# Performance work log

Hardware: AMD Instinct MI355X
Metric: run time of the kernel (lower is better)

## Reference

```python
import jax, jax.numpy as jnp
import numpy as np

DT = 0.05

def _conv(x, w):
    # x: [N,C,H,W], w: [O,I,kh,kw], SAME padding
    return jax.lax.conv_general_dilated(x, w, (1, 1), 'SAME',
                                        dimension_numbers=('NCHW', 'OIHW', 'NCHW'))

def _gru(h, x, wx, wh):
    # convolutional GRU cell (used for Bayesian jumps and SpatialGRU)
    xr, xz, xg = jnp.split(_conv(x, wx), 3, axis=1)
    hr, hz, hg = jnp.split(_conv(h, wh), 3, axis=1)
    r = jax.nn.sigmoid(xr + hr)
    z = jax.nn.sigmoid(xz + hz)
    g = jnp.tanh(xg + r * hg)
    return (1.0 - z) * h + z * g

def _ode_step(h, wrz, wg, dt):
    # GRU-ODE cell, explicit Euler: dh/dt = (1-z)*(g-h)
    r, z = jnp.split(jax.nn.sigmoid(_conv(h, wrz)), 2, axis=1)
    g = jnp.tanh(_conv(r * h, wg))
    return h + dt * (1.0 - z) * (g - h)

def _sgru(x, h0, wx, wh):
    # SpatialGRU: conv-GRU recurrence over the sequence dim
    def step(h, xt):
        h = _gru(h, xt, wx, wh)
        return h, h
    _, hs = jax.lax.scan(step, h0, x.transpose(1, 0, 2, 3, 4))
    return hs.transpose(1, 0, 2, 3, 4)

def setup_inputs() -> dict:
    key = jax.random.key(0)
    B, C, H, W = 2, 64, 64, 64
    Nc, Nl, NF = 3, 5, 6
    ks = jax.random.split(key, 16)
    f = lambda i, s: jax.random.normal(ks[i], s, jnp.float32)
    w = lambda i, s: 0.05 * jax.random.normal(ks[i], s, jnp.float32)
    inp = {}
    inp['future_prediction_input'] = f(0, (B, C, H, W))
    inp['camera_states'] = f(1, (B, Nc, C, H, W))
    inp['lidar_states'] = f(2, (B, Nl, C, H, W))
    # ragged obs times as exact multiples of DT; targets after all obs
    inp['camera_timestamp'] = jnp.broadcast_to(jnp.array([0., 2., 4.]) * DT, (B, Nc)).astype(jnp.float32)
    inp['lidar_timestamp'] = jnp.broadcast_to(jnp.array([1., 3., 5., 6., 7.]) * DT, (B, Nl)).astype(jnp.float32)
    inp['target_timestamp'] = jnp.broadcast_to(jnp.arange(8., 14.) * DT, (B, NF)).astype(jnp.float32)
    inp['ode_wrz'] = w(3, (2 * C, C, 3, 3))
    inp['ode_wg'] = w(4, (C, C, 3, 3))
    inp['jmp_wx'] = w(5, (3 * C, C, 3, 3))
    inp['jmp_wh'] = w(6, (3 * C, C, 3, 3))
    inp['sg0_wx'] = w(7, (3 * C, C, 3, 3))
    inp['sg0_wh'] = w(8, (3 * C, C, 3, 3))
    inp['sg1_wx'] = w(9, (3 * C, C, 3, 3))
    inp['sg1_wh'] = w(10, (3 * C, C, 3, 3))
    inp['res0_w1'] = w(11, (C, C, 3, 3))
    inp['res0_w2'] = w(12, (C, C, 3, 3))
    inp['dl_w1'] = w(13, (128, C, 3, 3))
    inp['dl_w2'] = w(14, (C, 128, 1, 1))
    return inp

def reference(future_prediction_input, camera_states, lidar_states,
              camera_timestamp, lidar_timestamp, target_timestamp,
              ode_wrz, ode_wg, jmp_wx, jmp_wh,
              sg0_wx, sg0_wh, sg1_wx, sg1_wh,
              res0_w1, res0_w2, dl_w1, dl_w2):
    dt = DT
    B, C, H, W = future_prediction_input.shape
    Nc, Nl, NF = camera_timestamp.shape[1], lidar_timestamp.shape[1], target_timestamp.shape[1]
    n_steps = Nc + Nl + NF  # static Euler grid covering all obs + target times
    # --- batched ragged merge: scatter obs onto the time grid (replaces per-sample dict sort) ---
    all_t = jnp.concatenate([camera_timestamp, lidar_timestamp], axis=1)          # [B, Nc+Nl]
    all_obs = jnp.concatenate([camera_states, lidar_states], axis=1)              # [B, Nc+Nl, C, H, W]
    steps = jnp.round(all_t / dt).astype(jnp.int32)
    bidx = jnp.arange(B)[:, None]
    grid = jnp.zeros((B, n_steps, C, H, W), all_obs.dtype).at[bidx, steps].set(all_obs)
    mask = jnp.zeros((B, n_steps), jnp.float32).at[bidx, steps].set(1.0)
    # --- ODE-RNN with Bayesian jumps: jump at obs, Euler-evolve between ---
    def ode_scan(h, xs):
        obs_t, m = xs
        hj = _gru(h, obs_t, jmp_wx, jmp_wh)
        h = jnp.where(m[:, None, None, None] > 0, hj, h)
        h = _ode_step(h, ode_wrz, ode_wg, dt)
        return h, h
    _, hs = jax.lax.scan(ode_scan, future_prediction_input,
                         (grid.transpose(1, 0, 2, 3, 4), mask.T))
    tsteps = jnp.round(target_timestamp / dt).astype(jnp.int32) - 1               # state after step k is time (k+1)*dt
    x = hs.transpose(1, 0, 2, 3, 4)[bidx, tsteps]                                 # [B, NF, C, H, W]
    auxilary_loss = jnp.float32(0.0)
    # --- spatial GRU stack + res blocks / DeepLab head ---
    hidden = x[:, 0]
    x = _sgru(x, hidden, sg0_wx, sg0_wh)
    xf = x.reshape(B * NF, C, H, W)
    xf = xf + _conv(jax.nn.relu(_conv(xf, res0_w1)), res0_w2)                     # residual Block
    x = xf.reshape(B, NF, C, H, W)
    x = _sgru(x, hidden, sg1_wx, sg1_wh)
    xf = x.reshape(B * NF, C, H, W)
    xf = _conv(jax.nn.relu(_conv(xf, dl_w1)), dl_w2)                              # DeepLabHead (3x3 -> relu -> 1x1)
    x = xf.reshape(B, NF, C, H, W)
    return (x, auxilary_loss)
```

## Files before the change

kernel.cpp:

```cpp
#include <hip/hip_runtime.h>
#include <stdint.h>

#define HWP 4096
#define SB  262144LL
#define FB  1572864LL
#define DTC 0.05f

typedef short short4v __attribute__((ext_vector_type(4)));
typedef short short8v __attribute__((ext_vector_type(8)));
typedef float f32x16  __attribute__((ext_vector_type(16)));

__device__ __forceinline__ float sigm(float x) { return 1.f / (1.f + __expf(-x)); }
__device__ __forceinline__ float tanhf_(float x) {
  float a = fabsf(x);
  float t = __expf(-2.f * a);
  float r = (1.f - t) / (1.f + t);
  return x < 0.f ? -r : r;
}
__device__ __forceinline__ float gru1(float h, float xr, float hr, float xz,
                                      float hz, float xg, float hg) {
  float r = sigm(xr + hr);
  float z = sigm(xz + hz);
  float g = tanhf_(xg + r * hg);
  return (1.f - z) * h + z * g;
}
__device__ __forceinline__ float b2f(unsigned int u) {
  return __uint_as_float(u << 16);
}
__device__ __forceinline__ unsigned short f2b(float f) {
  unsigned int x = __float_as_uint(f);
  unsigned int r = (x + 0x7fffu + ((x >> 16) & 1u)) >> 16;
  return (unsigned short)r;
}

struct WJobs {
  const float* src[11];
  unsigned short* dst[11];
  int oc[11];
  int blk_off[12];
};

__global__ __launch_bounds__(256) void convert_all(WJobs jobs)
{
  int b = blockIdx.x;
  int j = 0;
  while (b >= jobs.blk_off[j + 1]) ++j;
  int g = (b - jobs.blk_off[j]) * 256 + threadIdx.x;
  if (g >= jobs.oc[j] * 64) return;
  const float* w = jobs.src[j];
  unsigned short* dst = jobs.dst[j];
  int oc = g >> 6, ic = g & 63;
  int ocg = oc >> 5, m = oc & 31;
  int kh = ic >> 4, ks = (ic >> 3) & 1, jj = ic & 7;
  int lane = m + 32 * ks;
#pragma unroll
  for (int t = 0; t < 9; ++t) {
    float v = w[(size_t)(oc * 64 + ic) * 9 + t];
    unsigned short hi = f2b(v);
    unsigned short lo = f2b(v - b2f(hi));
    size_t fb = ((size_t)(ocg * 4 + kh) * 9 + t) * 1024;
    dst[fb + (size_t)lane * 8 + jj] = hi;
    dst[fb + 512 + (size_t)lane * 8 + jj] = lo;
  }
}

template<int NR>
__device__ __forceinline__ void stage_rows(
    unsigned short (*lds)[2][66][68], int slot0,
    const float* __restrict__ in_img, int gy0, int tid)
{
  int px = tid & 63, icq = tid >> 6;
  int ic0 = icq * 16;
  float v[NR][16];
#pragma unroll
  for (int r = 0; r < NR; ++r) {
    int gy = gy0 + r;
    if (gy >= 0 && gy < 64) {
#pragma unroll
      for (int i = 0; i < 16; ++i)
        v[r][i] = in_img[(size_t)(ic0 + i) * HWP + (size_t)gy * 64 + px];
    } else {
#pragma unroll
      for (int i = 0; i < 16; ++i) v[r][i] = 0.f;
    }
  }
#pragma unroll
  for (int r = 0; r < NR; ++r) {
    unsigned short hi[16], lo[16];
#pragma unroll
    for (int i = 0; i < 16; ++i) {
      hi[i] = f2b(v[r][i]);
      lo[i] = f2b(v[r][i] - b2f(hi[i]));
    }
    unsigned short* dhi = &lds[slot0 + r][0][px + 1][ic0];
    unsigned short* dlo = &lds[slot0 + r][1][px + 1][ic0];
#pragma unroll
    for (int q = 0; q < 4; ++q) {
      uint2 ph, pl;
      ph.x = (unsigned)hi[q*4+0] | ((unsigned)hi[q*4+1] << 16);
      ph.y = (unsigned)hi[q*4+2] | ((unsigned)hi[q*4+3] << 16);
      pl.x = (unsigned)lo[q*4+0] | ((unsigned)lo[q*4+1] << 16);
      pl.y = (unsigned)lo[q*4+2] | ((unsigned)lo[q*4+3] << 16);
      *(uint2*)&dhi[q*4] = ph;
      *(uint2*)&dlo[q*4] = pl;
    }
  }
}

#define LOAD_B_SLOT(SLOT, kx)                                                 \
  {                                                                           \
    const unsigned short* bph = &lds[SLOT][0][x0 + n + kx][khb];              \
    const unsigned short* bpl = &lds[SLOT][1][x0 + n + kx][khb];              \
    bhi.lo = *(const short4v*)bph; bhi.hi = *(const short4v*)(bph + 4);       \
    blo.lo = *(const short4v*)bpl; blo.hi = *(const short4v*)(bpl + 4);       \
  }

#define MFMA3(CACC, AHI, ALO)                                                 \
  CACC = __builtin_amdgcn_mfma_f32_32x32x16_bf16(AHI, bhi, CACC, 0, 0, 0);    \
  CACC = __builtin_amdgcn_mfma_f32_32x32x16_bf16(ALO, bhi, CACC, 0, 0, 0);    \
  CACC = __builtin_amdgcn_mfma_f32_32x32x16_bf16(AHI, blo, CACC, 0, 0, 0);

__global__ __launch_bounds__(256) void conv_mfma(
    const float* __restrict__ in_base, long long s1, long long s2,
    const float* __restrict__ cam, const float* __restrict__ lid, int s0,
    const unsigned short* __restrict__ wfrag, int OC,
    float* __restrict__ out_f32, unsigned short* __restrict__ out_b16,
    long long o1, long long o2, int flags)
{
  __shared__ __align__(16) unsigned short lds[4][2][66][68];

  int bpe = (OC >> 6) << 5;
  int bid = blockIdx.x;
  int e = bid / bpe; int r = bid - e * bpe;
  int ocb = r >> 5; int yb = r & 31;
  int y0 = yb << 1;
  int tid = threadIdx.x;
  int wv = tid >> 6, lane = tid & 63;
  int wocg = wv >> 1, wpx = wv & 1;
  int oc0w = ocb * 64 + wocg * 32;
  int x0 = wpx * 32;
  int n = lane & 31, ksub = lane >> 5;

  const float* in_img;
  if (cam) {
    int s = s0 + (e >> 1); int img = e & 1;
    int isLid = (0xEA >> s) & 1;
    int frm = isLid ? (s < 5 ? (s >> 1) : s - 3) : (s >> 1);
    in_img = isLid ? lid + ((size_t)img * 5 + frm) * SB
                   : cam + ((size_t)img * 3 + frm) * SB;
  } else {
    in_img = in_base + (size_t)(e >> 1) * s1 + (size_t)(e & 1) * s2;
  }
  size_t obase = (size_t)(e >> 1) * o1 + (size_t)(e & 1) * o2;

  for (int i = tid; i < 4488; i += 256)
    ((uint4*)lds)[i] = make_uint4(0u, 0u, 0u, 0u);
  __syncthreads();
  stage_rows<2>(lds, 0, in_img, y0 - 1, tid);
  stage_rows<2>(lds, 2, in_img, y0 + 1, tid);
  __syncthreads();

  size_t wfbase = (size_t)(oc0w >> 5) * 4;

  f32x16 c0, c1;
#pragma unroll
  for (int i = 0; i < 16; ++i) { c0[i] = 0.f; c1[i] = 0.f; }

#pragma unroll
  for (int kh = 0; kh < 4; ++kh) {
    int khb = kh * 16 + ksub * 8;
#pragma unroll
    for (int kidx = 0; kidx < 9; ++kidx) {
      int ky = kidx / 3, kx = kidx - ky * 3;
      const unsigned short* ap =
          wfrag + ((wfbase + kh) * 9 + kidx) * 1024 + (size_t)lane * 8;
      short8v ahi = *(const short8v*)ap;
      short8v alo = *(const short8v*)(ap + 512);
      short8v bhi, blo;
      LOAD_B_SLOT(ky, kx);
      MFMA3(c0, ahi, alo);
      LOAD_B_SLOT(ky + 1, kx);
      MFMA3(c1, ahi, alo);
    }
  }

  auto epilogue = [&](const f32x16& c, int y) {
#pragma unroll
    for (int reg = 0; reg < 16; ++reg) {
      int row = (reg & 3) + 8 * (reg >> 2) + 4 * ksub;
      int oc = oc0w + row;
      float v = c[reg];
      if (flags & 1) v = fmaxf(v, 0.f);
      size_t off = obase + (size_t)oc * HWP + (size_t)y * 64 + (x0 + n);
      if (out_b16) {
        out_b16[off] = f2b(v);
      } else {
        if (flags & 2) v += out_f32[off];
        out_f32[off] = v;
      }
    }
  };
  epilogue(c0, y0);
  epilogue(c1, y0 + 1);
}

__global__ __launch_bounds__(256) void gru_mfma(
    const float* __restrict__ hprev, long long h_is,
    const unsigned short* __restrict__ wfrag,
    const unsigned short* __restrict__ xcs,
    float* __restrict__ hout, long long o_is)
{
  __shared__ __align__(16) unsigned short lds[3][2][66][68];
  int bid = blockIdx.x;
  int img = bid >> 6, y = bid & 63;
  int tid = threadIdx.x;
  int wv = tid >> 6, lane = tid & 63;
  int wchg = wv >> 1, wpx = wv & 1;
  int x0 = wpx * 32;
  int n = lane & 31, ksub = lane >> 5;

  const float* in_img = hprev + (size_t)img * h_is;
  for (int i = tid; i < 3366; i += 256)
    ((uint4*)lds)[i] = make_uint4(0u, 0u, 0u, 0u);
  __syncthreads();
  stage_rows<3>(lds, 0, in_img, y - 1, tid);
  __syncthreads();

  f32x16 cr, cz, cg;
#pragma unroll
  for (int i = 0; i < 16; ++i) { cr[i] = 0.f; cz[i] = 0.f; cg[i] = 0.f; }

#pragma unroll
  for (int kh = 0; kh < 4; ++kh) {
    int khb = kh * 16 + ksub * 8;
#pragma unroll
    for (int kidx = 0; kidx < 9; ++kidx) {
      int ky = kidx / 3, kx = kidx - ky * 3;
      short8v bhi, blo;
      LOAD_B_SLOT(ky, kx);
      const unsigned short* apr =
          wfrag + (((size_t)wchg * 4 + kh) * 9 + kidx) * 1024 + (size_t)lane * 8;
      const unsigned short* apz = apr + (size_t)2 * 4 * 9 * 1024;
      const unsigned short* apg = apr + (size_t)4 * 4 * 9 * 1024;
      short8v arh = *(const short8v*)apr;
      short8v arl = *(const short8v*)(apr + 512);
      short8v azh = *(const short8v*)apz;
      short8v azl = *(const short8v*)(apz + 512);
      short8v agh = *(const short8v*)apg;
      short8v agl = *(const short8v*)(apg + 512);
      MFMA3(cr, arh, arl);
      MFMA3(cz, azh, azl);
      MFMA3(cg, agh, agl);
    }
  }

  const unsigned short* xcb = xcs + (size_t)img * 786432;
#pragma unroll
  for (int reg = 0; reg < 16; ++reg) {
    int crow = (reg & 3) + 8 * (reg >> 2) + 4 * ksub;
    int c = wchg * 32 + crow;
    size_t px = (size_t)y * 64 + x0 + n;
    float xr = b2f(xcb[(size_t)c * HWP + px]);
    float xz = b2f(xcb[(size_t)(c + 64) * HWP + px]);
    float xg = b2f(xcb[(size_t)(c + 128) * HWP + px]);
    float hv = hprev[(size_t)img * h_is + (size_t)c * HWP + px];
    hout[(size_t)img * o_is + (size_t)c * HWP + px] =
        gru1(hv, xr, cr[reg], xz, cz[reg], xg, cg[reg]);
  }
}

__global__ __launch_bounds__(256) void rz_mfma(
    const float* __restrict__ hbuf,
    const unsigned short* __restrict__ wfrag,
    float* __restrict__ rhb, float* __restrict__ zsb)
{
  __shared__ __align__(16) unsigned short lds[3][2][66][68];
  int bid = blockIdx.x;
  int img = bid >> 6, y = bid & 63;
  int tid = threadIdx.x;
  int wv = tid >> 6, lane = tid & 63;
  int wchg = wv >> 1, wpx = wv & 1;
  int x0 = wpx * 32;
  int n = lane & 31, ksub = lane >> 5;

  const float* in_img = hbuf + (size_t)img * SB;
  for (int i = tid; i < 3366; i += 256)
    ((uint4*)lds)[i] = make_uint4(0u, 0u, 0u, 0u);
  __syncthreads();
  stage_rows<3>(lds, 0, in_img, y - 1, tid);
  __syncthreads();

  f32x16 cr, cz;
#pragma unroll
  for (int i = 0; i < 16; ++i) { cr[i] = 0.f; cz[i] = 0.f; }

#pragma unroll
  for (int kh = 0; kh < 4; ++kh) {
    int khb = kh * 16 + ksub * 8;
#pragma unroll
    for (int kidx = 0; kidx < 9; ++kidx) {
      int ky = kidx / 3, kx = kidx - ky * 3;
      short8v bhi, blo;
      LOAD_B_SLOT(ky, kx);
      const unsigned short* apr =
          wfrag + (((size_t)wchg * 4 + kh) * 9 + kidx) * 1024 + (size_t)lane * 8;
      const unsigned short* apz = apr + (size_t)2 * 4 * 9 * 1024;
      short8v arh = *(const short8v*)apr;
      short8v arl = *(const short8v*)(apr + 512);
      short8v azh = *(const short8v*)apz;
      short8v azl = *(const short8v*)(apz + 512);
      MFMA3(cr, arh, arl);
      MFMA3(cz, azh, azl);
    }
  }

#pragma unroll
  for (int reg = 0; reg < 16; ++reg) {
    int crow = (reg & 3) + 8 * (reg >> 2) + 4 * ksub;
    int c = wchg * 32 + crow;
    size_t idx = (size_t)img * SB + (size_t)c * HWP + (size_t)y * 64 + x0 + n;
    rhb[idx] = sigm(cr[reg]) * hbuf[idx];
    zsb[idx] = sigm(cz[reg]);
  }
}

__global__ __launch_bounds__(256) void odeg_mfma(
    const float* __restrict__ rhb,
    const unsigned short* __restrict__ wfrag,
    const float* __restrict__ zsb,
    const float* __restrict__ hsrc, float* __restrict__ hdst,
    float* __restrict__ fr, float* __restrict__ hid)
{
  __shared__ __align__(16) unsigned short lds[3][2][66][68];
  int bid = blockIdx.x;
  int img = bid >> 6, y = bid & 63;
  int tid = threadIdx.x;
  int wv = tid >> 6, lane = tid & 63;
  int wchg = wv >> 1, wpx = wv & 1;
  int x0 = wpx * 32;
  int n = lane & 31, ksub = lane >> 5;

  const float* in_img = rhb + (size_t)img * SB;
  for (int i = tid; i < 3366; i += 256)
    ((uint4*)lds)[i] = make_uint4(0u, 0u, 0u, 0u);
  __syncthreads();
  stage_rows<3>(lds, 0, in_img, y - 1, tid);
  __syncthreads();

  f32x16 cg;
#pragma unroll
  for (int i = 0; i < 16; ++i) cg[i] = 0.f;

#pragma unroll
  for (int kh = 0; kh < 4; ++kh) {
    int khb = kh * 16 + ksub * 8;
#pragma unroll
    for (int kidx = 0; kidx < 9; ++kidx) {
      int ky = kidx / 3, kx = kidx - ky * 3;
      short8v bhi, blo;
      LOAD_B_SLOT(ky, kx);
      const unsigned short* ap =
          wfrag + (((size_t)wchg * 4 + kh) * 9 + kidx) * 1024 + (size_t)lane * 8;
      short8v ahi = *(const short8v*)ap;
      short8v alo = *(const short8v*)(ap + 512);
      MFMA3(cg, ahi, alo);
    }
  }

#pragma unroll
  for (int reg = 0; reg < 16; ++reg) {
    int crow = (reg & 3) + 8 * (reg >> 2) + 4 * ksub;
    int c = wchg * 32 + crow;
    size_t px = (size_t)y * 64 + x0 + n;
    size_t idx = (size_t)img * SB + (size_t)c * HWP + px;
    float z = zsb[idx];
    float h = hsrc[idx];
    float o = h + DTC * (1.f - z) * (tanhf_(cg[reg]) - h);
    hdst[idx] = o;
    if (fr)  fr[(size_t)img * FB + (size_t)c * HWP + px] = o;
    if (hid) hid[idx] = o;
  }
}

__global__ __launch_bounds__(256) void conv1x1_k(
    const unsigned short* __restrict__ in, const float* __restrict__ wt,
    float* __restrict__ out)
{
  int bid = blockIdx.x;
  int img = bid >> 5; int r = bid & 31; int pxb = r >> 3; int ocg = r & 7;
  int px = pxb * 1024 + threadIdx.x * 4;
  const unsigned short* ip = in + (size_t)img * 128 * HWP + px;
  float4 acc[8] = {};
  for (int ic = 0; ic < 128; ++ic) {
    ushort4 u = *(const ushort4*)&ip[(size_t)ic * HWP];
    float4 v;
    v.x = b2f(u.x); v.y = b2f(u.y); v.z = b2f(u.z); v.w = b2f(u.w);
#pragma unroll
    for (int j = 0; j < 8; ++j) {
      float w = wt[(ocg * 8 + j) * 128 + ic];
      acc[j].x += v.x * w; acc[j].y += v.y * w;
      acc[j].z += v.z * w; acc[j].w += v.w * w;
    }
  }
#pragma unroll
  for (int j = 0; j < 8; ++j) {
    int oc = ocg * 8 + j;
    float* dst = out + ((size_t)img * 64 + oc) * HWP + px;
    *(float4*)dst = acc[j];
  }
}

__global__ __launch_bounds__(256) void copy_k(
    const float* __restrict__ in, float* __restrict__ out)
{
  int i = blockIdx.x * 256 + threadIdx.x;
  ((float4*)out)[i] = ((const float4*)in)[i];
}

__global__ void aux_k(float* out) { out[0] = 0.f; }

extern "C" void kernel_launch(void* const* d_in, const int* in_sizes, int n_in,
                              void* d_out, int out_size, void* d_ws, size_t ws_size,
                              hipStream_t stream)
{
  const float* fpi = (const float*)d_in[0];
  const float* cam = (const float*)d_in[1];
  const float* lid = (const float*)d_in[2];
  const float* w_ode_rz = (const float*)d_in[6];
  const float* w_ode_g  = (const float*)d_in[7];
  const float* w_jmp_x  = (const float*)d_in[8];
  const float* w_jmp_h  = (const float*)d_in[9];
  const float* w_sg0_x  = (const float*)d_in[10];
  const float* w_sg0_h  = (const float*)d_in[11];
  const float* w_sg1_x  = (const float*)d_in[12];
  const float* w_sg1_h  = (const float*)d_in[13];
  const float* w_res_1  = (const float*)d_in[14];
  const float* w_res_2  = (const float*)d_in[15];
  const float* w_dl_1   = (const float*)d_in[16];
  const float* w_dl_2   = (const float*)d_in[17];

  float* ws     = (float*)d_ws;
  float* frames = ws;
  float* hidden = ws + 3145728;
  float* h_a    = ws + 3670016;
  float* h_b    = ws + 4194304;
  float* rhb    = ws + 4718592;
  float* zsb    = ws + 5242880;
  unsigned short* xcu    = (unsigned short*)(ws + 5505024);
  unsigned short* wbuf   = (unsigned short*)(ws + 7864320);
  float* big_res = ws + 3670016;
  unsigned short* big_dl = (unsigned short*)(ws + 3670016);

  const long long SLABU = 1572864;
  unsigned short* wjx  = wbuf;
  unsigned short* ws0x = wbuf + 221184;
  unsigned short* ws1x = wbuf + 442368;
  unsigned short* wre1 = wbuf + 663552;
  unsigned short* wre2 = wbuf + 737280;
  unsigned short* wdl1 = wbuf + 811008;
  unsigned short* wjh  = wbuf + 958464;
  unsigned short* ws0h = wbuf + 1179648;
  unsigned short* ws1h = wbuf + 1400832;
  unsigned short* wrz  = wbuf + 1622016;
  unsigned short* wg   = wbuf + 1769472;

  WJobs jobs;
  const float* srcs[11] = {w_jmp_x, w_sg0_x, w_sg1_x, w_jmp_h, w_sg0_h, w_sg1_h,
                           w_dl_1, w_ode_rz, w_res_1, w_res_2, w_ode_g};
  unsigned short* dsts[11] = {wjx, ws0x, ws1x, wjh, ws0h, ws1h,
                              wdl1, wrz, wre1, wre2, wg};
  int ocs[11] = {192, 192, 192, 192, 192, 192, 128, 128, 64, 64, 64};
  int off = 0;
  for (int j = 0; j < 11; ++j) {
    jobs.src[j] = srcs[j]; jobs.dst[j] = dsts[j]; jobs.oc[j] = ocs[j];
    jobs.blk_off[j] = off; off += ocs[j] / 4;
  }
  jobs.blk_off[11] = off;
  convert_all<<<off, 256, 0, stream>>>(jobs);

  copy_k<<<512, 256, 0, stream>>>(fpi, h_a);

  const int batch_s0[3] = {0, 3, 6};
  const int batch_n[3]  = {3, 3, 2};
  for (int b = 0; b < 3; ++b) {
    conv_mfma<<<batch_n[b] * 2 * 3 * 32, 256, 0, stream>>>(
        nullptr, 0, 0, cam, lid, batch_s0[b], wjx, 192,
        nullptr, xcu, SLABU, 786432, 0);
    for (int tl = 0; tl < batch_n[b]; ++tl) {
      int t = batch_s0[b] + tl;
      gru_mfma<<<128, 256, 0, stream>>>(h_a, SB, wjh,
                                        xcu + (long long)tl * SLABU, h_b, SB);
      rz_mfma<<<128, 256, 0, stream>>>(h_b, wrz, rhb, zsb);
      float* fr  = (t >= 7) ? frames + (long long)(t - 7) * SB : nullptr;
      float* hid = (t == 7) ? hidden : nullptr;
      odeg_mfma<<<128, 256, 0, stream>>>(rhb, wg, zsb, h_b, h_a, fr, hid);
    }
  }
  for (int t = 8; t < 13; ++t) {
    rz_mfma<<<128, 256, 0, stream>>>(h_a, wrz, rhb, zsb);
    odeg_mfma<<<128, 256, 0, stream>>>(rhb, wg, zsb, h_a, h_a,
                                       frames + (long long)(t - 7) * SB, nullptr);
  }

  for (int b = 0; b < 2; ++b) {
    conv_mfma<<<576, 256, 0, stream>>>(frames + (long long)(b * 3) * SB, SB, FB,
                                       nullptr, nullptr, 0, ws0x, 192,
                                       nullptr, xcu, SLABU, 786432, 0);
    for (int tl = 0; tl < 3; ++tl) {
      int f = b * 3 + tl;
      const float* hp = (f == 0) ? hidden : frames + (long long)(f - 1) * SB;
      long long hbs = (f == 0) ? SB : FB;
      gru_mfma<<<128, 256, 0, stream>>>(hp, hbs, ws0h,
                                        xcu + (long long)tl * SLABU,
                                        frames + (long long)f * SB, FB);
    }
  }

  conv_mfma<<<384, 256, 0, stream>>>(frames, 2 * SB, SB, nullptr, nullptr, 0,
                                     wre1, 64, big_res, nullptr, 2 * SB, SB, 1);
  conv_mfma<<<384, 256, 0, stream>>>(big_res, 2 * SB, SB, nullptr, nullptr, 0,
                                     wre2, 64, frames, nullptr, 2 * SB, SB, 2);

  for (int b = 0; b < 2; ++b) {
    conv_mfma<<<576, 256, 0, stream>>>(frames + (long long)(b * 3) * SB, SB, FB,
                                       nullptr, nullptr, 0, ws1x, 192,
                                       nullptr, xcu, SLABU, 786432, 0);
    for (int tl = 0; tl < 3; ++tl) {
      int f = b * 3 + tl;
      const float* hp = (f == 0) ? hidden : frames + (long long)(f - 1) * SB;
      long long hbs = (f == 0) ? SB : FB;
      gru_mfma<<<128, 256, 0, stream>>>(hp, hbs, ws1h,
                                        xcu + (long long)tl * SLABU,
                                        frames + (long long)f * SB, FB);
    }
  }

  conv_mfma<<<768, 256, 0, stream>>>(frames, 2 * SB, SB, nullptr, nullptr, 0,
                                     wdl1, 128, nullptr, big_dl,
                                     1048576, 524288, 1);
  conv1x1_k<<<384, 256, 0, stream>>>(big_dl, w_dl_2, (float*)d_out);

  aux_k<<<1, 1, 0, stream>>>((float*)d_out + 3145728);
}
```

Before: 1.278 ms.

## Fuse recurrent GRU/ODE step kernels into persistent kernel with grid barriers

Replaces the many small per-timestep gru/rz/odeg kernel launches with one persistent kernel per scan segment. The segment runs 128 blocks and synchronises between dependent stages with an atomic-counter grid barrier. LDS zeroing is reduced to clearing only the halo columns once per block. This targets launch overhead and inter-kernel gaps across roughly 40 small launches. The barrier assumes all 128 blocks are co-resident (not a cooperative launch) and adds spin-wait cost plus a memset per segment.

```diff
diff --git a/kernel.cpp b/kernel.cpp
--- a/kernel.cpp
+++ b/kernel.cpp
@@ -4,7 +4,9 @@
 #define HWP 4096
 #define SB  262144LL
 #define FB  1572864LL
+#define SLABU 1572864LL
 #define DTC 0.05f
+#define NBLK 128u
 
 typedef short short4v __attribute__((ext_vector_type(4)));
 typedef short short8v __attribute__((ext_vector_type(8)));
@@ -31,6 +33,23 @@
   unsigned int x = __float_as_uint(f);
   unsigned int r = (x + 0x7fffu + ((x >> 16) & 1u)) >> 16;
   return (unsigned short)r;
+}
+
+__device__ __forceinline__ void grid_barrier(unsigned int* ctr,
+                                             unsigned int* s_phase)
+{
+  __syncthreads();
+  if (threadIdx.x == 0) {
+    unsigned int ph = ++(*s_phase);
+    __threadfence();
+    __hip_atomic_fetch_add(ctr, 1u, __ATOMIC_RELAXED, __HIP_MEMORY_SCOPE_AGENT);
+    while (__hip_atomic_load(ctr, __ATOMIC_RELAXED, __HIP_MEMORY_SCOPE_AGENT)
+           < ph * NBLK) {
+      __builtin_amdgcn_s_sleep(1);
+    }
+    __threadfence();
+  }
+  __syncthreads();
 }
 
 struct WJobs {
@@ -64,6 +83,19 @@
   }
 }
 
+__device__ __forceinline__ void zero_halo(
+    unsigned short (*lds)[2][66][68], int nslots, int tid)
+{
+  int tot = nslots * 4 * 16;
+  if (tid < tot) {
+    int row = tid >> 4, q = tid & 15;
+    int slot = row >> 2, rem = row & 3;
+    int plane = rem >> 1;
+    int col = (rem & 1) ? 65 : 0;
+    ((uint2*)&lds[slot][plane][col][0])[q] = make_uint2(0u, 0u);
+  }
+}
+
 template<int NR>
 __device__ __forceinline__ void stage_rows(
     unsigned short (*lds)[2][66][68], int slot0,
@@ -120,109 +152,18 @@
   CACC = __builtin_amdgcn_mfma_f32_32x32x16_bf16(ALO, bhi, CACC, 0, 0, 0);    \
   CACC = __builtin_amdgcn_mfma_f32_32x32x16_bf16(AHI, blo, CACC, 0, 0, 0);
 
-__global__ __launch_bounds__(256) void conv_mfma(
-    const float* __restrict__ in_base, long long s1, long long s2,
-    const float* __restrict__ cam, const float* __restrict__ lid, int s0,
-    const unsigned short* __restrict__ wfrag, int OC,
-    float* __restrict__ out_f32, unsigned short* __restrict__ out_b16,
-    long long o1, long long o2, int flags)
-{
-  __shared__ __align__(16) unsigned short lds[4][2][66][68];
-
-  int bpe = (OC >> 6) << 5;
-  int bid = blockIdx.x;
-  int e = bid / bpe; int r = bid - e * bpe;
-  int ocb = r >> 5; int yb = r & 31;
-  int y0 = yb << 1;
-  int tid = threadIdx.x;
-  int wv = tid >> 6, lane = tid & 63;
-  int wocg = wv >> 1, wpx = wv & 1;
-  int oc0w = ocb * 64 + wocg * 32;
-  int x0 = wpx * 32;
-  int n = lane & 31, ksub = lane >> 5;
-
-  const float* in_img;
-  if (cam) {
-    int s = s0 + (e >> 1); int img = e & 1;
-    int isLid = (0xEA >> s) & 1;
-    int frm = isLid ? (s < 5 ? (s >> 1) : s - 3) : (s >> 1);
-    in_img = isLid ? lid + ((size_t)img * 5 + frm) * SB
-                   : cam + ((size_t)img * 3 + frm) * SB;
-  } else {
-    in_img = in_base + (size_t)(e >> 1) * s1 + (size_t)(e & 1) * s2;
-  }
-  size_t obase = (size_t)(e >> 1) * o1 + (size_t)(e & 1) * o2;
-
-  for (int i = tid; i < 4488; i += 256)
-    ((uint4*)lds)[i] = make_uint4(0u, 0u, 0u, 0u);
-  __syncthreads();
-  stage_rows<2>(lds, 0, in_img, y0 - 1, tid);
-  stage_rows<2>(lds, 2, in_img, y0 + 1, tid);
-  __syncthreads();
-
-  size_t wfbase = (size_t)(oc0w >> 5) * 4;
-
-  f32x16 c0, c1;
-#pragma unroll
-  for (int i = 0; i < 16; ++i) { c0[i] = 0.f; c1[i] = 0.f; }
-
-#pragma unroll
-  for (int kh = 0; kh < 4; ++kh) {
-    int khb = kh * 16 + ksub * 8;
-#pragma unroll
-    for (int kidx = 0; kidx < 9; ++kidx) {
-      int ky = kidx / 3, kx = kidx - ky * 3;
-      const unsigned short* ap =
-          wfrag + ((wfbase + kh) * 9 + kidx) * 1024 + (size_t)lane * 8;
-      short8v ahi = *(const short8v*)ap;
-      short8v alo = *(const short8v*)(ap + 512);
-      short8v bhi, blo;
-      LOAD_B_SLOT(ky, kx);
-      MFMA3(c0, ahi, alo);
-      LOAD_B_SLOT(ky + 1, kx);
-      MFMA3(c1, ahi, alo);
-    }
-  }
-
-  auto epilogue = [&](const f32x16& c, int y) {
-#pragma unroll
-    for (int reg = 0; reg < 16; ++reg) {
-      int row = (reg & 3) + 8 * (reg >> 2) + 4 * ksub;
-      int oc = oc0w + row;
-      float v = c[reg];
-      if (flags & 1) v = fmaxf(v, 0.f);
-      size_t off = obase + (size_t)oc * HWP + (size_t)y * 64 + (x0 + n);
-      if (out_b16) {
-        out_b16[off] = f2b(v);
-      } else {
-        if (flags & 2) v += out_f32[off];
-        out_f32[off] = v;
-      }
-    }
-  };
-  epilogue(c0, y0);
-  epilogue(c1, y0 + 1);
-}
-
-__global__ __launch_bounds__(256) void gru_mfma(
-    const float* __restrict__ hprev, long long h_is,
-    const unsigned short* __restrict__ wfrag,
-    const unsigned short* __restrict__ xcs,
-    float* __restrict__ hout, long long o_is)
-{
-  __shared__ __align__(16) unsigned short lds[3][2][66][68];
-  int bid = blockIdx.x;
-  int img = bid >> 6, y = bid & 63;
-  int tid = threadIdx.x;
+__device__ void st_gru(unsigned short (*lds)[2][66][68], int img, int y, int tid,
+                       const float* __restrict__ hprev, long long h_is,
+                       const unsigned short* __restrict__ wfrag,
+                       const unsigned short* __restrict__ xcs,
+                       float* __restrict__ hout, long long o_is)
+{
   int wv = tid >> 6, lane = tid & 63;
   int wchg = wv >> 1, wpx = wv & 1;
   int x0 = wpx * 32;
   int n = lane & 31, ksub = lane >> 5;
 
   const float* in_img = hprev + (size_t)img * h_is;
-  for (int i = tid; i < 3366; i += 256)
-    ((uint4*)lds)[i] = make_uint4(0u, 0u, 0u, 0u);
-  __syncthreads();
   stage_rows<3>(lds, 0, in_img, y - 1, tid);
   __syncthreads();
 
@@ -269,24 +210,17 @@
   }
 }
 
-__global__ __launch_bounds__(256) void rz_mfma(
-    const float* __restrict__ hbuf,
-    const unsigned short* __restrict__ wfrag,
-    float* __restrict__ rhb, float* __restrict__ zsb)
-{
-  __shared__ __align__(16) unsigned short lds[3][2][66][68];
-  int bid = blockIdx.x;
-  int img = bid >> 6, y = bid & 63;
-  int tid = threadIdx.x;
+__device__ void st_rz(unsigned short (*lds)[2][66][68], int img, int y, int tid,
+                      const float* __restrict__ hbuf,
+                      const unsigned short* __restrict__ wfrag,
+                      float* __restrict__ rhb, float* __restrict__ zsb)
+{
   int wv = tid >> 6, lane = tid & 63;
   int wchg = wv >> 1, wpx = wv & 1;
   int x0 = wpx * 32;
   int n = lane & 31, ksub = lane >> 5;
 
   const float* in_img = hbuf + (size_t)img * SB;
-  for (int i = tid; i < 3366; i += 256)
-    ((uint4*)lds)[i] = make_uint4(0u, 0u, 0u, 0u);
-  __syncthreads();
   stage_rows<3>(lds, 0, in_img, y - 1, tid);
   __syncthreads();
 
@@ -324,26 +258,19 @@
   }
 }
 
-__global__ __launch_bounds__(256) void odeg_mfma(
-    const float* __restrict__ rhb,
-    const unsigned short* __restrict__ wfrag,
-    const float* __restrict__ zsb,
-    const float* __restrict__ hsrc, float* __restrict__ hdst,
-    float* __restrict__ fr, float* __restrict__ hid)
-{
-  __shared__ __align__(16) unsigned short lds[3][2][66][68];
-  int bid = blockIdx.x;
-  int img = bid >> 6, y = bid & 63;
-  int tid = threadIdx.x;
+__device__ void st_odeg(unsigned short (*lds)[2][66][68], int img, int y, int tid,
+                        const float* __restrict__ rhb,
+                        const unsigned short* __restrict__ wfrag,
+                        const float* __restrict__ zsb,
+                        const float* __restrict__ hsrc, float* __restrict__ hdst,
+                        float* __restrict__ fr, float* __restrict__ hid)
+{
   int wv = tid >> 6, lane = tid & 63;
   int wchg = wv >> 1, wpx = wv & 1;
   int x0 = wpx * 32;
   int n = lane & 31, ksub = lane >> 5;
 
   const float* in_img = rhb + (size_t)img * SB;
-  for (int i = tid; i < 3366; i += 256)
-    ((uint4*)lds)[i] = make_uint4(0u, 0u, 0u, 0u);
-  __syncthreads();
   stage_rows<3>(lds, 0, in_img, y - 1, tid);
   __syncthreads();
 
@@ -380,6 +307,136 @@
     if (fr)  fr[(size_t)img * FB + (size_t)c * HWP + px] = o;
     if (hid) hid[idx] = o;
   }
+}
+
+__global__ __launch_bounds__(256) void coop_scan(
+    int mode, int t0, int t1,
+    const unsigned short* wh, const unsigned short* wrz,
+    const unsigned short* wg, const unsigned short* xcu,
+    float* h_a, float* h_b, float* rhb, float* zsb,
+    float* frames, float* hidden, unsigned int* ctr)
+{
+  __shared__ __align__(16) unsigned short lds[3][2][66][68];
+  __shared__ unsigned int s_phase;
+  int tid = threadIdx.x;
+  int bid = blockIdx.x;
+  int img = bid >> 6, y = bid & 63;
+
+  if (tid == 0) s_phase = 0u;
+  zero_halo(lds, 3, tid);
+  __syncthreads();
+
+  if (mode == 0) {
+    for (int t = t0; t < t1; ++t) {
+      const float* hsrc;
+      if (t < 8) {
+        st_gru(lds, img, y, tid, h_a, SB, wh,
+               xcu + (size_t)(t - t0) * SLABU, h_b, SB);
+        grid_barrier(ctr, &s_phase);
+        hsrc = h_b;
+      } else {
+        hsrc = h_a;
+      }
+      st_rz(lds, img, y, tid, hsrc, wrz, rhb, zsb);
+      grid_barrier(ctr, &s_phase);
+      float* fr  = (t >= 7) ? frames + (size_t)(t - 7) * SB : nullptr;
+      float* hid = (t == 7) ? hidden : nullptr;
+      st_odeg(lds, img, y, tid, rhb, wg, zsb, hsrc, h_a, fr, hid);
+      if (t < t1 - 1) grid_barrier(ctr, &s_phase);
+    }
+  } else {
+    for (int f = t0; f < t1; ++f) {
+      const float* hp = (f == 0) ? hidden : frames + (size_t)(f - 1) * SB;
+      long long hbs = (f == 0) ? SB : FB;
+      st_gru(lds, img, y, tid, hp, hbs, wh,
+             xcu + (size_t)(f - t0) * SLABU, frames + (size_t)f * SB, FB);
+      if (f < t1 - 1) grid_barrier(ctr, &s_phase);
+    }
+  }
+}
+
+__global__ __launch_bounds__(256) void conv_mfma(
+    const float* __restrict__ in_base, long long s1, long long s2,
+    const float* __restrict__ cam, const float* __restrict__ lid, int s0,
+    const unsigned short* __restrict__ wfrag, int OC,
+    float* __restrict__ out_f32, unsigned short* __restrict__ out_b16,
+    long long o1, long long o2, int flags)
+{
+  __shared__ __align__(16) unsigned short lds[4][2][66][68];
+
+  int bpe = (OC >> 6) << 5;
+  int bid = blockIdx.x;
+  int e = bid / bpe; int r = bid - e * bpe;
+  int ocb = r >> 5; int yb = r & 31;
+  int y0 = yb << 1;
+  int tid = threadIdx.x;
+  int wv = tid >> 6, lane = tid & 63;
+  int wocg = wv >> 1, wpx = wv & 1;
+  int oc0w = ocb * 64 + wocg * 32;
+  int x0 = wpx * 32;
+  int n = lane & 31, ksub = lane >> 5;
+
+  const float* in_img;
+  if (cam) {
+    int s = s0 + (e >> 1); int img = e & 1;
+    int isLid = (0xEA >> s) & 1;
+    int frm = isLid ? (s < 5 ? (s >> 1) : s - 3) : (s >> 1);
+    in_img = isLid ? lid + ((size_t)img * 5 + frm) * SB
+                   : cam + ((size_t)img * 3 + frm) * SB;
+  } else {
+    in_img = in_base + (size_t)(e >> 1) * s1 + (size_t)(e & 1) * s2;
+  }
+  size_t obase = (size_t)(e >> 1) * o1 + (size_t)(e & 1) * o2;
+
+  for (int i = tid; i < 4488; i += 256)
+    ((uint4*)lds)[i] = make_uint4(0u, 0u, 0u, 0u);
+  __syncthreads();
+  stage_rows<2>(lds, 0, in_img, y0 - 1, tid);
+  stage_rows<2>(lds, 2, in_img, y0 + 1, tid);
+  __syncthreads();
+
+  size_t wfbase = (size_t)(oc0w >> 5) * 4;
+
+  f32x16 c0, c1;
+#pragma unroll
+  for (int i = 0; i < 16; ++i) { c0[i] = 0.f; c1[i] = 0.f; }
+
+#pragma unroll
+  for (int kh = 0; kh < 4; ++kh) {
+    int khb = kh * 16 + ksub * 8;
+#pragma unroll
+    for (int kidx = 0; kidx < 9; ++kidx) {
+      int ky = kidx / 3, kx = kidx - ky * 3;
+      const unsigned short* ap =
+          wfrag + ((wfbase + kh) * 9 + kidx) * 1024 + (size_t)lane * 8;
+      short8v ahi = *(const short8v*)ap;
+      short8v alo = *(const short8v*)(ap + 512);
+      short8v bhi, blo;
+      LOAD_B_SLOT(ky, kx);
+      MFMA3(c0, ahi, alo);
+      LOAD_B_SLOT(ky + 1, kx);
+      MFMA3(c1, ahi, alo);
+    }
+  }
+
+  auto epilogue = [&](const f32x16& c, int y) {
+#pragma unroll
+    for (int reg = 0; reg < 16; ++reg) {
+      int row = (reg & 3) + 8 * (reg >> 2) + 4 * ksub;
+      int oc = oc0w + row;
+      float v = c[reg];
+      if (flags & 1) v = fmaxf(v, 0.f);
+      size_t off = obase + (size_t)oc * HWP + (size_t)y * 64 + (x0 + n);
+      if (out_b16) {
+        out_b16[off] = f2b(v);
+      } else {
+        if (flags & 2) v += out_f32[off];
+        out_f32[off] = v;
+      }
+    }
+  };
+  epilogue(c0, y0);
+  epilogue(c1, y0 + 1);
 }
 
 __global__ __launch_bounds__(256) void conv1x1_k(
@@ -450,8 +507,8 @@
   unsigned short* wbuf   = (unsigned short*)(ws + 7864320);
   float* big_res = ws + 3670016;
   unsigned short* big_dl = (unsigned short*)(ws + 3670016);
-
-  const long long SLABU = 1572864;
+  unsigned int* ctr = (unsigned int*)(ws + 8785920);
+
   unsigned short* wjx  = wbuf;
   unsigned short* ws0x = wbuf + 221184;
   unsigned short* ws1x = wbuf + 442368;
@@ -480,40 +537,27 @@
 
   copy_k<<<512, 256, 0, stream>>>(fpi, h_a);
 
+  auto scan = [&](int mode, int a, int b, unsigned short* whp) {
+    hipMemsetAsync(ctr, 0, 4, stream);
+    coop_scan<<<NBLK, 256, 0, stream>>>(mode, a, b, whp, wrz, wg, xcu,
+                                        h_a, h_b, rhb, zsb, frames, hidden, ctr);
+  };
+
   const int batch_s0[3] = {0, 3, 6};
   const int batch_n[3]  = {3, 3, 2};
+  const int batch_t1[3] = {3, 6, 13};
   for (int b = 0; b < 3; ++b) {
     conv_mfma<<<batch_n[b] * 2 * 3 * 32, 256, 0, stream>>>(
         nullptr, 0, 0, cam, lid, batch_s0[b], wjx, 192,
         nullptr, xcu, SLABU, 786432, 0);
-    for (int tl = 0; tl < batch_n[b]; ++tl) {
-      int t = batch_s0[b] + tl;
-      gru_mfma<<<128, 256, 0, stream>>>(h_a, SB, wjh,
-                                        xcu + (long long)tl * SLABU, h_b, SB);
-      rz_mfma<<<128, 256, 0, stream>>>(h_b, wrz, rhb, zsb);
-      float* fr  = (t >= 7) ? frames + (long long)(t - 7) * SB : nullptr;
-      float* hid = (t == 7) ? hidden : nullptr;
-      odeg_mfma<<<128, 256, 0, stream>>>(rhb, wg, zsb, h_b, h_a, fr, hid);
-    }
-  }
-  for (int t = 8; t < 13; ++t) {
-    rz_mfma<<<128, 256, 0, stream>>>(h_a, wrz, rhb, zsb);
-    odeg_mfma<<<128, 256, 0, stream>>>(rhb, wg, zsb, h_a, h_a,
-                                       frames + (long long)(t - 7) * SB, nullptr);
+    scan(0, batch_s0[b], batch_t1[b], wjh);
   }
 
   for (int b = 0; b < 2; ++b) {
     conv_mfma<<<576, 256, 0, stream>>>(frames + (long long)(b * 3) * SB, SB, FB,
                                        nullptr, nullptr, 0, ws0x, 192,
                                        nullptr, xcu, SLABU, 786432, 0);
-    for (int tl = 0; tl < 3; ++tl) {
-      int f = b * 3 + tl;
-      const float* hp = (f == 0) ? hidden : frames + (long long)(f - 1) * SB;
-      long long hbs = (f == 0) ? SB : FB;
-      gru_mfma<<<128, 256, 0, stream>>>(hp, hbs, ws0h,
-                                        xcu + (long long)tl * SLABU,
-                                        frames + (long long)f * SB, FB);
-    }
+    scan(1, b * 3, b * 3 + 3, ws0h);
   }
 
   conv_mfma<<<384, 256, 0, stream>>>(frames, 2 * SB, SB, nullptr, nullptr, 0,
@@ -525,14 +569,7 @@
     conv_mfma<<<576, 256, 0, stream>>>(frames + (long long)(b * 3) * SB, SB, FB,
                                        nullptr, nullptr, 0, ws1x, 192,
                                        nullptr, xcu, SLABU, 786432, 0);
-    for (int tl = 0; tl < 3; ++tl) {
-      int f = b * 3 + tl;
-      const float* hp = (f == 0) ? hidden : frames + (long long)(f - 1) * SB;
-      long long hbs = (f == 0) ? SB : FB;
-      gru_mfma<<<128, 256, 0, stream>>>(hp, hbs, ws1h,
-                                        xcu + (long long)tl * SLABU,
-                                        frames + (long long)f * SB, FB);
-    }
+    scan(1, b * 3, b * 3 + 3, ws1h);
   }
 
   conv_mfma<<<768, 256, 0, stream>>>(frames, 2 * SB, SB, nullptr, nullptr, 0,
```

Measured after the change: 2.255 ms. +76.4%, slower.

## Fuse ODE r/z conv and g conv into one kernel with halo recompute

Applied to the files above, without the earlier changes.

Merges the rz_mfma and odeg_mfma kernels into a single rzodeg_mfma kernel. Each block recomputes the r-gate for the neighbouring rows (y-1, y+1) so that r*h for the 3x3 g-convolution can be built in LDS, with no global round trip through the rhb/zsb buffers. This halves the kernel launches per ODE step and removes the intermediate global traffic. In exchange the r-conv MFMA work per block triples, and register pressure rises from four accumulators. Pure ODE steps now ping-pong between h_a and h_b because source and destination can no longer alias.

```diff
diff --git a/kernel.cpp b/kernel.cpp
--- a/kernel.cpp
+++ b/kernel.cpp
@@ -4,6 +4,7 @@
 #define HWP 4096
 #define SB  262144LL
 #define FB  1572864LL
+#define SLABU 1572864LL
 #define DTC 0.05f
 
 typedef short short4v __attribute__((ext_vector_type(4)));
@@ -119,90 +120,6 @@
   CACC = __builtin_amdgcn_mfma_f32_32x32x16_bf16(AHI, bhi, CACC, 0, 0, 0);    \
   CACC = __builtin_amdgcn_mfma_f32_32x32x16_bf16(ALO, bhi, CACC, 0, 0, 0);    \
   CACC = __builtin_amdgcn_mfma_f32_32x32x16_bf16(AHI, blo, CACC, 0, 0, 0);
-
-__global__ __launch_bounds__(256) void conv_mfma(
-    const float* __restrict__ in_base, long long s1, long long s2,
-    const float* __restrict__ cam, const float* __restrict__ lid, int s0,
-    const unsigned short* __restrict__ wfrag, int OC,
-    float* __restrict__ out_f32, unsigned short* __restrict__ out_b16,
-    long long o1, long long o2, int flags)
-{
-  __shared__ __align__(16) unsigned short lds[4][2][66][68];
-
-  int bpe = (OC >> 6) << 5;
-  int bid = blockIdx.x;
-  int e = bid / bpe; int r = bid - e * bpe;
-  int ocb = r >> 5; int yb = r & 31;
-  int y0 = yb << 1;
-  int tid = threadIdx.x;
-  int wv = tid >> 6, lane = tid & 63;
-  int wocg = wv >> 1, wpx = wv & 1;
-  int oc0w = ocb * 64 + wocg * 32;
-  int x0 = wpx * 32;
-  int n = lane & 31, ksub = lane >> 5;
-
-  const float* in_img;
-  if (cam) {
-    int s = s0 + (e >> 1); int img = e & 1;
-    int isLid = (0xEA >> s) & 1;
-    int frm = isLid ? (s < 5 ? (s >> 1) : s - 3) : (s >> 1);
-    in_img = isLid ? lid + ((size_t)img * 5 + frm) * SB
-                   : cam + ((size_t)img * 3 + frm) * SB;
-  } else {
-    in_img = in_base + (size_t)(e >> 1) * s1 + (size_t)(e & 1) * s2;
-  }
-  size_t obase = (size_t)(e >> 1) * o1 + (size_t)(e & 1) * o2;
-
-  for (int i = tid; i < 4488; i += 256)
-    ((uint4*)lds)[i] = make_uint4(0u, 0u, 0u, 0u);
-  __syncthreads();
-  stage_rows<2>(lds, 0, in_img, y0 - 1, tid);
-  stage_rows<2>(lds, 2, in_img, y0 + 1, tid);
-  __syncthreads();
-
-  size_t wfbase = (size_t)(oc0w >> 5) * 4;
-
-  f32x16 c0, c1;
-#pragma unroll
-  for (int i = 0; i < 16; ++i) { c0[i] = 0.f; c1[i] = 0.f; }
-
-#pragma unroll
-  for (int kh = 0; kh < 4; ++kh) {
-    int khb = kh * 16 + ksub * 8;
-#pragma unroll
-    for (int kidx = 0; kidx < 9; ++kidx) {
-      int ky = kidx / 3, kx = kidx - ky * 3;
-      const unsigned short* ap =
-          wfrag + ((wfbase + kh) * 9 + kidx) * 1024 + (size_t)lane * 8;
-      short8v ahi = *(const short8v*)ap;
-      short8v alo = *(const short8v*)(ap + 512);
-      short8v bhi, blo;
-      LOAD_B_SLOT(ky, kx);
-      MFMA3(c0, ahi, alo);
-      LOAD_B_SLOT(ky + 1, kx);
-      MFMA3(c1, ahi, alo);
-    }
-  }
-
-  auto epilogue = [&](const f32x16& c, int y) {
-#pragma unroll
-    for (int reg = 0; reg < 16; ++reg) {
-      int row = (reg & 3) + 8 * (reg >> 2) + 4 * ksub;
-      int oc = oc0w + row;
-      float v = c[reg];
-      if (flags & 1) v = fmaxf(v, 0.f);
-      size_t off = obase + (size_t)oc * HWP + (size_t)y * 64 + (x0 + n);
-      if (out_b16) {
-        out_b16[off] = f2b(v);
-      } else {
-        if (flags & 2) v += out_f32[off];
-        out_f32[off] = v;
-      }
-    }
-  };
-  epilogue(c0, y0);
-  epilogue(c1, y0 + 1);
-}
 
 __global__ __launch_bounds__(256) void gru_mfma(
     const float* __restrict__ hprev, long long h_is,
@@ -269,12 +186,14 @@
   }
 }
 
-__global__ __launch_bounds__(256) void rz_mfma(
-    const float* __restrict__ hbuf,
-    const unsigned short* __restrict__ wfrag,
-    float* __restrict__ rhb, float* __restrict__ zsb)
-{
-  __shared__ __align__(16) unsigned short lds[3][2][66][68];
+__global__ __launch_bounds__(256) void rzodeg_mfma(
+    const float* __restrict__ hsrc,
+    const unsigned short* __restrict__ wrzf,
+    const unsigned short* __restrict__ wgf,
+    float* __restrict__ hdst,
+    float* __restrict__ fr, float* __restrict__ hid)
+{
+  __shared__ __align__(16) unsigned short lds[5][2][66][68];
   int bid = blockIdx.x;
   int img = bid >> 6, y = bid & 63;
   int tid = threadIdx.x;
@@ -283,16 +202,21 @@
   int x0 = wpx * 32;
   int n = lane & 31, ksub = lane >> 5;
 
-  const float* in_img = hbuf + (size_t)img * SB;
-  for (int i = tid; i < 3366; i += 256)
-    ((uint4*)lds)[i] = make_uint4(0u, 0u, 0u, 0u);
-  __syncthreads();
-  stage_rows<3>(lds, 0, in_img, y - 1, tid);
-  __syncthreads();
-
-  f32x16 cr, cz;
-#pragma unroll
-  for (int i = 0; i < 16; ++i) { cr[i] = 0.f; cz[i] = 0.f; }
+  for (int i = tid; i < 5 * 4 * 16; i += 256) {
+    int row = i >> 4, q = i & 15;
+    int slot = row >> 2, rem = row & 3;
+    int plane = rem >> 1;
+    int col = (rem & 1) ? 65 : 0;
+    ((uint2*)&lds[slot][plane][col][0])[q] = make_uint2(0u, 0u);
+  }
+  const float* in_img = hsrc + (size_t)img * SB;
+  stage_rows<3>(lds, 0, in_img, y - 2, tid);
+  stage_rows<2>(lds, 3, in_img, y + 1, tid);
+  __syncthreads();
+
+  f32x16 cr0, cr1, cr2, cz;
+#pragma unroll
+  for (int i = 0; i < 16; ++i) { cr0[i]=0.f; cr1[i]=0.f; cr2[i]=0.f; cz[i]=0.f; }
 
 #pragma unroll
   for (int kh = 0; kh < 4; ++kh) {
@@ -300,17 +224,60 @@
 #pragma unroll
     for (int kidx = 0; kidx < 9; ++kidx) {
       int ky = kidx / 3, kx = kidx - ky * 3;
-      short8v bhi, blo;
-      LOAD_B_SLOT(ky, kx);
       const unsigned short* apr =
-          wfrag + (((size_t)wchg * 4 + kh) * 9 + kidx) * 1024 + (size_t)lane * 8;
+          wrzf + (((size_t)wchg * 4 + kh) * 9 + kidx) * 1024 + (size_t)lane * 8;
       const unsigned short* apz = apr + (size_t)2 * 4 * 9 * 1024;
       short8v arh = *(const short8v*)apr;
       short8v arl = *(const short8v*)(apr + 512);
       short8v azh = *(const short8v*)apz;
       short8v azl = *(const short8v*)(apz + 512);
-      MFMA3(cr, arh, arl);
-      MFMA3(cz, azh, azl);
+      { short8v bhi, blo; LOAD_B_SLOT(ky, kx);     MFMA3(cr0, arh, arl); }
+      { short8v bhi, blo; LOAD_B_SLOT(ky + 1, kx); MFMA3(cr1, arh, arl);
+                                                   MFMA3(cz,  azh, azl); }
+      { short8v bhi, blo; LOAD_B_SLOT(ky + 2, kx); MFMA3(cr2, arh, arl); }
+    }
+  }
+
+  __syncthreads();
+
+  {
+    int pxc = x0 + n;
+#pragma unroll
+    for (int reg = 0; reg < 16; ++reg) {
+      int crow = (reg & 3) + 8 * (reg >> 2) + 4 * ksub;
+      int c = wchg * 32 + crow;
+      const float* hc = hsrc + (size_t)img * SB + (size_t)c * HWP;
+      float rv0 = (y - 1 >= 0)
+          ? sigm(cr0[reg]) * hc[(size_t)(y - 1) * 64 + pxc] : 0.f;
+      float rv1 = sigm(cr1[reg]) * hc[(size_t)y * 64 + pxc];
+      float rv2 = (y + 1 < 64)
+          ? sigm(cr2[reg]) * hc[(size_t)(y + 1) * 64 + pxc] : 0.f;
+      unsigned short h0 = f2b(rv0), l0 = f2b(rv0 - b2f(h0));
+      unsigned short h1 = f2b(rv1), l1 = f2b(rv1 - b2f(h1));
+      unsigned short h2 = f2b(rv2), l2 = f2b(rv2 - b2f(h2));
+      lds[0][0][pxc + 1][c] = h0; lds[0][1][pxc + 1][c] = l0;
+      lds[1][0][pxc + 1][c] = h1; lds[1][1][pxc + 1][c] = l1;
+      lds[2][0][pxc + 1][c] = h2; lds[2][1][pxc + 1][c] = l2;
+    }
+  }
+  __syncthreads();
+
+  f32x16 cg;
+#pragma unroll
+  for (int i = 0; i < 16; ++i) cg[i] = 0.f;
+#pragma unroll
+  for (int kh = 0; kh < 4; ++kh) {
+    int khb = kh * 16 + ksub * 8;
+#pragma unroll
+    for (int kidx = 0; kidx < 9; ++kidx) {
+      int ky = kidx / 3, kx = kidx - ky * 3;
+      const unsigned short* ap =
+          wgf + (((size_t)wchg * 4 + kh) * 9 + kidx) * 1024 + (size_t)lane * 8;
+      short8v ahi = *(const short8v*)ap;
+      short8v alo = *(const short8v*)(ap + 512);
+      short8v bhi, blo;
+      LOAD_B_SLOT(ky, kx);
+      MFMA3(cg, ahi, alo);
     }
   }
 
@@ -318,68 +285,99 @@
   for (int reg = 0; reg < 16; ++reg) {
     int crow = (reg & 3) + 8 * (reg >> 2) + 4 * ksub;
     int c = wchg * 32 + crow;
-    size_t idx = (size_t)img * SB + (size_t)c * HWP + (size_t)y * 64 + x0 + n;
-    rhb[idx] = sigm(cr[reg]) * hbuf[idx];
-    zsb[idx] = sigm(cz[reg]);
-  }
-}
-
-__global__ __launch_bounds__(256) void odeg_mfma(
-    const float* __restrict__ rhb,
-    const unsigned short* __restrict__ wfrag,
-    const float* __restrict__ zsb,
-    const float* __restrict__ hsrc, float* __restrict__ hdst,
-    float* __restrict__ fr, float* __restrict__ hid)
-{
-  __shared__ __align__(16) unsigned short lds[3][2][66][68];
-  int bid = blockIdx.x;
-  int img = bid >> 6, y = bid & 63;
-  int tid = threadIdx.x;
-  int wv = tid >> 6, lane = tid & 63;
-  int wchg = wv >> 1, wpx = wv & 1;
-  int x0 = wpx * 32;
-  int n = lane & 31, ksub = lane >> 5;
-
-  const float* in_img = rhb + (size_t)img * SB;
-  for (int i = tid; i < 3366; i += 256)
-    ((uint4*)lds)[i] = make_uint4(0u, 0u, 0u, 0u);
-  __syncthreads();
-  stage_rows<3>(lds, 0, in_img, y - 1, tid);
-  __syncthreads();
-
-  f32x16 cg;
-#pragma unroll
-  for (int i = 0; i < 16; ++i) cg[i] = 0.f;
-
-#pragma unroll
-  for (int kh = 0; kh < 4; ++kh) {
-    int khb = kh * 16 + ksub * 8;
-#pragma unroll
-    for (int kidx = 0; kidx < 9; ++kidx) {
-      int ky = kidx / 3, kx = kidx - ky * 3;
-      short8v bhi, blo;
-      LOAD_B_SLOT(ky, kx);
-      const unsigned short* ap =
-          wfrag + (((size_t)wchg * 4 + kh) * 9 + kidx) * 1024 + (size_t)lane * 8;
-      short8v ahi = *(const short8v*)ap;
-      short8v alo = *(const short8v*)(ap + 512);
-      MFMA3(cg, ahi, alo);
-    }
-  }
-
-#pragma unroll
-  for (int reg = 0; reg < 16; ++reg) {
-    int crow = (reg & 3) + 8 * (reg >> 2) + 4 * ksub;
-    int c = wchg * 32 + crow;
-    size_t px = (size_t)y * 64 + x0 + n;
-    size_t idx = (size_t)img * SB + (size_t)c * HWP + px;
-    float z = zsb[idx];
+    size_t pxo = (size_t)y * 64 + x0 + n;
+    size_t idx = (size_t)img * SB + (size_t)c * HWP + pxo;
+    float z = sigm(cz[reg]);
     float h = hsrc[idx];
     float o = h + DTC * (1.f - z) * (tanhf_(cg[reg]) - h);
     hdst[idx] = o;
-    if (fr)  fr[(size_t)img * FB + (size_t)c * HWP + px] = o;
+    if (fr)  fr[(size_t)img * FB + (size_t)c * HWP + pxo] = o;
     if (hid) hid[idx] = o;
   }
+}
+
+__global__ __launch_bounds__(256) void conv_mfma(
+    const float* __restrict__ in_base, long long s1, long long s2,
+    const float* __restrict__ cam, const float* __restrict__ lid, int s0,
+    const unsigned short* __restrict__ wfrag, int OC,
+    float* __restrict__ out_f32, unsigned short* __restrict__ out_b16,
+    long long o1, long long o2, int flags)
+{
+  __shared__ __align__(16) unsigned short lds[4][2][66][68];
+
+  int bpe = (OC >> 6) << 5;
+  int bid = blockIdx.x;
+  int e = bid / bpe; int r = bid - e * bpe;
+  int ocb = r >> 5; int yb = r & 31;
+  int y0 = yb << 1;
+  int tid = threadIdx.x;
+  int wv = tid >> 6, lane = tid & 63;
+  int wocg = wv >> 1, wpx = wv & 1;
+  int oc0w = ocb * 64 + wocg * 32;
+  int x0 = wpx * 32;
+  int n = lane & 31, ksub = lane >> 5;
+
+  const float* in_img;
+  if (cam) {
+    int s = s0 + (e >> 1); int img = e & 1;
+    int isLid = (0xEA >> s) & 1;
+    int frm = isLid ? (s < 5 ? (s >> 1) : s - 3) : (s >> 1);
+    in_img = isLid ? lid + ((size_t)img * 5 + frm) * SB
+                   : cam + ((size_t)img * 3 + frm) * SB;
+  } else {
+    in_img = in_base + (size_t)(e >> 1) * s1 + (size_t)(e & 1) * s2;
+  }
+  size_t obase = (size_t)(e >> 1) * o1 + (size_t)(e & 1) * o2;
+
+  for (int i = tid; i < 4488; i += 256)
+    ((uint4*)lds)[i] = make_uint4(0u, 0u, 0u, 0u);
+  __syncthreads();
+  stage_rows<2>(lds, 0, in_img, y0 - 1, tid);
+  stage_rows<2>(lds, 2, in_img, y0 + 1, tid);
+  __syncthreads();
+
+  size_t wfbase = (size_t)(oc0w >> 5) * 4;
+
+  f32x16 c0, c1;
+#pragma unroll
+  for (int i = 0; i < 16; ++i) { c0[i] = 0.f; c1[i] = 0.f; }
+
+#pragma unroll
+  for (int kh = 0; kh < 4; ++kh) {
+    int khb = kh * 16 + ksub * 8;
+#pragma unroll
+    for (int kidx = 0; kidx < 9; ++kidx) {
+      int ky = kidx / 3, kx = kidx - ky * 3;
+      const unsigned short* ap =
+          wfrag + ((wfbase + kh) * 9 + kidx) * 1024 + (size_t)lane * 8;
+      short8v ahi = *(const short8v*)ap;
+      short8v alo = *(const short8v*)(ap + 512);
+      short8v bhi, blo;
+      LOAD_B_SLOT(ky, kx);
+      MFMA3(c0, ahi, alo);
+      LOAD_B_SLOT(ky + 1, kx);
+      MFMA3(c1, ahi, alo);
+    }
+  }
+
+  auto epilogue = [&](const f32x16& c, int y) {
+#pragma unroll
+    for (int reg = 0; reg < 16; ++reg) {
+      int row = (reg & 3) + 8 * (reg >> 2) + 4 * ksub;
+      int oc = oc0w + row;
+      float v = c[reg];
+      if (flags & 1) v = fmaxf(v, 0.f);
+      size_t off = obase + (size_t)oc * HWP + (size_t)y * 64 + (x0 + n);
+      if (out_b16) {
+        out_b16[off] = f2b(v);
+      } else {
+        if (flags & 2) v += out_f32[off];
+        out_f32[off] = v;
+      }
+    }
+  };
+  epilogue(c0, y0);
+  epilogue(c1, y0 + 1);
 }
 
 __global__ __launch_bounds__(256) void conv1x1_k(
@@ -444,14 +442,11 @@
   float* hidden = ws + 3145728;
   float* h_a    = ws + 3670016;
   float* h_b    = ws + 4194304;
-  float* rhb    = ws + 4718592;
-  float* zsb    = ws + 5242880;
   unsigned short* xcu    = (unsigned short*)(ws + 5505024);
   unsigned short* wbuf   = (unsigned short*)(ws + 7864320);
   float* big_res = ws + 3670016;
   unsigned short* big_dl = (unsigned short*)(ws + 3670016);
 
-  const long long SLABU = 1572864;
   unsigned short* wjx  = wbuf;
   unsigned short* ws0x = wbuf + 221184;
   unsigned short* ws1x = wbuf + 442368;
@@ -481,25 +476,27 @@
   copy_k<<<512, 256, 0, stream>>>(fpi, h_a);
 
   const int batch_s0[3] = {0, 3, 6};
-  const int batch_n[3]  = {3, 3, 2};
+  const int batch_t1[3] = {3, 6, 13};
+  float* cur = h_a;
   for (int b = 0; b < 3; ++b) {
-    conv_mfma<<<batch_n[b] * 2 * 3 * 32, 256, 0, stream>>>(
+    int nobs = (b < 2) ? 3 : 2;
+    conv_mfma<<<nobs * 2 * 3 * 32, 256, 0, stream>>>(
         nullptr, 0, 0, cam, lid, batch_s0[b], wjx, 192,
         nullptr, xcu, SLABU, 786432, 0);
-    for (int tl = 0; tl < batch_n[b]; ++tl) {
-      int t = batch_s0[b] + tl;
-      gru_mfma<<<128, 256, 0, stream>>>(h_a, SB, wjh,
-                                        xcu + (long long)tl * SLABU, h_b, SB);
-      rz_mfma<<<128, 256, 0, stream>>>(h_b, wrz, rhb, zsb);
+    for (int t = batch_s0[b]; t < batch_t1[b]; ++t) {
       float* fr  = (t >= 7) ? frames + (long long)(t - 7) * SB : nullptr;
       float* hid = (t == 7) ? hidden : nullptr;
-      odeg_mfma<<<128, 256, 0, stream>>>(rhb, wg, zsb, h_b, h_a, fr, hid);
-    }
-  }
-  for (int t = 8; t < 13; ++t) {
-    rz_mfma<<<128, 256, 0, stream>>>(h_a, wrz, rhb, zsb);
-    odeg_mfma<<<128, 256, 0, stream>>>(rhb, wg, zsb, h_a, h_a,
-                                       frames + (long long)(t - 7) * SB, nullptr);
+      if (t < 8) {
+        gru_mfma<<<128, 256, 0, stream>>>(
+            h_a, SB, wjh, xcu + (long long)(t - batch_s0[b]) * SLABU, h_b, SB);
+        rzodeg_mfma<<<128, 256, 0, stream>>>(h_b, wrz, wg, h_a, fr, hid);
+        cur = h_a;
+      } else {
+        float* dst = (cur == h_a) ? h_b : h_a;
+        rzodeg_mfma<<<128, 256, 0, stream>>>(cur, wrz, wg, dst, fr, nullptr);
+        cur = dst;
+      }
+    }
   }
 
   for (int b = 0; b < 2; ++b) {
```

After: 1.197 ms. 6.4% less time.
